# Optimization experiments

Measured on AMD Instinct MI355X. Metric: run time of the kernel, lower is better.

The kernel has to match this reference:

```python
import jax, jax.numpy as jnp
import numpy as np

# Rook contiguity: down, up, right, left
ROOK = ((1, 0), (-1, 0), (0, 1), (0, -1))


def setup_inputs() -> dict:
    key = jax.random.key(0)
    H = W = 2048
    activities = jnp.ones((H, W), dtype=bool)
    vertex_weights = jax.random.uniform(key, (H, W), dtype=jnp.float32)
    return {"activities": activities, "vertex_weights": vertex_weights}


def reference(activities, vertex_weights):
    """Faithful jit-safe translation of GridGraph.get_adjacency_matrix.

    Returns the COO triplet (values, rows, cols) of the adjacency matrix of
    shape (N, N) with N = number of active vertices. All vertices are active
    (activities is all-ones), so N == H*W and the 4*N candidate-edge layout is
    static; invalid edges (out of bounds / inactive target) are masked to
    value 0 at index (0, 0) — an explicit zero, semantically a no-op in COO.
    """
    H, W = activities.shape
    flat = activities.ravel()
    # active_map: passive (i,j) -> active vertex index (== coord_to_active_vertex_index)
    order = jnp.cumsum(flat.astype(jnp.int32)) - 1
    active_map = jnp.where(flat, order, -1).reshape(H, W)
    # source coordinates of active vertices (all active -> full grid, row-major)
    ii, jj = jnp.meshgrid(jnp.arange(H), jnp.arange(W), indexing="ij")
    si, sj = ii.ravel(), jj.ravel()          # [N]
    src_idx = active_map[si, sj]             # [N] == arange(N)

    rows_l, cols_l, vals_l = [], [], []
    for di, dj in ROOK:  # static 4-way loop over neighbor directions
        ci, cj = si + di, sj + dj
        inb = (ci >= 0) & (ci < H) & (cj >= 0) & (cj < W)
        cic = jnp.clip(ci, 0, H - 1)
        cjc = jnp.clip(cj, 0, W - 1)
        valid = inb & activities[cic, cjc]   # edge_validity
        rows_l.append(jnp.where(valid, src_idx, 0))
        cols_l.append(jnp.where(valid, active_map[cic, cjc], 0))
        vals_l.append(jnp.where(valid, vertex_weights[cic, cjc], jnp.float32(0.0)))

    values = jnp.concatenate(vals_l)   # [4N]
    rows = jnp.concatenate(rows_l)     # [4N]
    cols = jnp.concatenate(cols_l)     # [4N]
    return values, rows, cols
```

## Files before the change

kernel.cpp:

```cpp
#include <hip/hip_runtime.h>


constexpr int HH = 2048;
constexpr int WW = 2048;
constexpr long long NN = (long long)HH * WW;

__global__ __launch_bounds__(1024) void grid_adj_kernel(
    const float* __restrict__ w, float* __restrict__ out)
{
    const int t = blockIdx.x * blockDim.x + threadIdx.x;
    const int p = t << 2;
    const int i = p >> 11;
    const int j = p & (WW - 1);

    float* __restrict__ vals = out;
    float* __restrict__ rows = out + 4 * NN;
    float* __restrict__ cols = out + 8 * NN;

    const float fp = (float)p;
    const float4 pf = make_float4(fp, fp + 1.f, fp + 2.f, fp + 3.f);
    const float4 z4 = make_float4(0.f, 0.f, 0.f, 0.f);

    const float4 c0 = *(const float4*)(w + p);

    {
        float4 v = z4, r = z4, c = z4;
        if (i + 1 < HH) {
            v = *(const float4*)(w + p + WW);
            r = pf;
            const float fq = fp + (float)WW;
            c = make_float4(fq, fq + 1.f, fq + 2.f, fq + 3.f);
        }
        *(float4*)(vals + p) = v;
        *(float4*)(rows + p) = r;
        *(float4*)(cols + p) = c;
    }

    {
        float4 v = z4, r = z4, c = z4;
        if (i >= 1) {
            v = *(const float4*)(w + p - WW);
            r = pf;
            const float fq = fp - (float)WW;
            c = make_float4(fq, fq + 1.f, fq + 2.f, fq + 3.f);
        }
        const long long o = NN + p;
        *(float4*)(vals + o) = v;
        *(float4*)(rows + o) = r;
        *(float4*)(cols + o) = c;
    }

    {
        const bool lastok = (j < WW - 4);
        float w4 = 0.f, r3 = 0.f, c3 = 0.f;
        if (lastok) {
            w4 = w[p + 4];
            r3 = fp + 3.f;
            c3 = fp + 4.f;
        }
        const long long o = 2 * NN + p;
        *(float4*)(vals + o) = make_float4(c0.y, c0.z, c0.w, w4);
        *(float4*)(rows + o) = make_float4(pf.x, pf.y, pf.z, r3);
        *(float4*)(cols + o) = make_float4(fp + 1.f, fp + 2.f, fp + 3.f, c3);
    }

    {
        const bool firstok = (j > 0);
        float wm1 = 0.f, r0 = 0.f, c0e = 0.f;
        if (firstok) {
            wm1 = w[p - 1];
            r0 = fp;
            c0e = fp - 1.f;
        }
        const long long o = 3 * NN + p;
        *(float4*)(vals + o) = make_float4(wm1, c0.x, c0.y, c0.z);
        *(float4*)(rows + o) = make_float4(r0, pf.y, pf.z, pf.w);
        *(float4*)(cols + o) = make_float4(c0e, fp, fp + 1.f, fp + 2.f);
    }
}

extern "C" void kernel_launch(void* const* d_in, const int* in_sizes, int n_in,
                              void* d_out, int out_size, void* d_ws, size_t ws_size,
                              hipStream_t stream) {
    const float* w = (const float*)d_in[1];
    float* out = (float*)d_out;

    const int threads = 1024;
    const int total_threads = (int)(NN / 4);
    const int blocks = total_threads / threads;
    grid_adj_kernel<<<blocks, threads, 0, stream>>>(w, out);
}
```

Measured before the change: 213.0 us.

## Assign each block to a single output stream instead of writing all twelve

The kernel is restructured so each block writes one of the twelve output segments (vals, rows and cols for each of four directions), with each thread covering four float4 chunks. Before, every thread wrote to twelve widely separated addresses. Now each wavefront streams contiguously into one region, which is meant to improve DRAM write locality and cut the number of concurrently open streams. In exchange the weight array is re-read by the four value-segment blocks, and the per-segment branching is uniform within a block.

New measurement: 212.1 us. Within noise of the previous version (-0.4%).

```diff
diff --git a/kernel.cpp b/kernel.cpp
--- a/kernel.cpp
+++ b/kernel.cpp
@@ -3,79 +3,67 @@
 
 constexpr int HH = 2048;
 constexpr int WW = 2048;
-constexpr long long NN = (long long)HH * WW;
+constexpr int NN = HH * WW;
 
-__global__ __launch_bounds__(1024) void grid_adj_kernel(
+__global__ __launch_bounds__(1024) void grid_adj_stream(
     const float* __restrict__ w, float* __restrict__ out)
 {
-    const int t = blockIdx.x * blockDim.x + threadIdx.x;
-    const int p = t << 2;
-    const int i = p >> 11;
-    const int j = p & (WW - 1);
+    const int s   = blockIdx.x >> 8;
+    const int blk = blockIdx.x & 255;
+    const int a   = s >> 2;
+    const int d   = s & 3;
+    (void)a;
 
-    float* __restrict__ vals = out;
-    float* __restrict__ rows = out + 4 * NN;
-    float* __restrict__ cols = out + 8 * NN;
+    float* __restrict__ dst = out + (long long)s * NN;
 
-    const float fp = (float)p;
-    const float4 pf = make_float4(fp, fp + 1.f, fp + 2.f, fp + 3.f);
-    const float4 z4 = make_float4(0.f, 0.f, 0.f, 0.f);
+#pragma unroll
+    for (int it = 0; it < 4; ++it) {
+        const int p = ((blk << 2) + it) * 4096 + ((int)threadIdx.x << 2);
+        const int j = p & (WW - 1);
+        const float fp = (float)p;
+        float4 r = make_float4(0.f, 0.f, 0.f, 0.f);
 
-    const float4 c0 = *(const float4*)(w + p);
+        if (d == 0) {
+            if (p < NN - WW) {
+                if (s == 0)      r = *(const float4*)(w + p + WW);
+                else if (s == 4) r = make_float4(fp, fp + 1.f, fp + 2.f, fp + 3.f);
+                else {           const float fq = fp + (float)WW;
+                                 r = make_float4(fq, fq + 1.f, fq + 2.f, fq + 3.f); }
+            }
+        } else if (d == 1) {
+            if (p >= WW) {
+                if (s == 1)      r = *(const float4*)(w + p - WW);
+                else if (s == 5) r = make_float4(fp, fp + 1.f, fp + 2.f, fp + 3.f);
+                else {           const float fq = fp - (float)WW;
+                                 r = make_float4(fq, fq + 1.f, fq + 2.f, fq + 3.f); }
+            }
+        } else if (d == 2) {
+            const bool lastok = (j < WW - 4);
+            if (s == 2) {
+                const float4 c0 = *(const float4*)(w + p);
+                float w4 = 0.f;
+                if (lastok) w4 = w[p + 4];
+                r = make_float4(c0.y, c0.z, c0.w, w4);
+            } else if (s == 6) {
+                r = make_float4(fp, fp + 1.f, fp + 2.f, lastok ? fp + 3.f : 0.f);
+            } else {
+                r = make_float4(fp + 1.f, fp + 2.f, fp + 3.f, lastok ? fp + 4.f : 0.f);
+            }
+        } else {
+            const bool firstok = (j > 0);
+            if (s == 3) {
+                const float4 c0 = *(const float4*)(w + p);
+                float wm1 = 0.f;
+                if (firstok) wm1 = w[p - 1];
+                r = make_float4(wm1, c0.x, c0.y, c0.z);
+            } else if (s == 7) {
+                r = make_float4(firstok ? fp : 0.f, fp + 1.f, fp + 2.f, fp + 3.f);
+            } else {
+                r = make_float4(firstok ? fp - 1.f : 0.f, fp, fp + 1.f, fp + 2.f);
+            }
+        }
 
-    {
-        float4 v = z4, r = z4, c = z4;
-        if (i + 1 < HH) {
-            v = *(const float4*)(w + p + WW);
-            r = pf;
-            const float fq = fp + (float)WW;
-            c = make_float4(fq, fq + 1.f, fq + 2.f, fq + 3.f);
-        }
-        *(float4*)(vals + p) = v;
-        *(float4*)(rows + p) = r;
-        *(float4*)(cols + p) = c;
-    }
-
-    {
-        float4 v = z4, r = z4, c = z4;
-        if (i >= 1) {
-            v = *(const float4*)(w + p - WW);
-            r = pf;
-            const float fq = fp - (float)WW;
-            c = make_float4(fq, fq + 1.f, fq + 2.f, fq + 3.f);
-        }
-        const long long o = NN + p;
-        *(float4*)(vals + o) = v;
-        *(float4*)(rows + o) = r;
-        *(float4*)(cols + o) = c;
-    }
-
-    {
-        const bool lastok = (j < WW - 4);
-        float w4 = 0.f, r3 = 0.f, c3 = 0.f;
-        if (lastok) {
-            w4 = w[p + 4];
-            r3 = fp + 3.f;
-            c3 = fp + 4.f;
-        }
-        const long long o = 2 * NN + p;
-        *(float4*)(vals + o) = make_float4(c0.y, c0.z, c0.w, w4);
-        *(float4*)(rows + o) = make_float4(pf.x, pf.y, pf.z, r3);
-        *(float4*)(cols + o) = make_float4(fp + 1.f, fp + 2.f, fp + 3.f, c3);
-    }
-
-    {
-        const bool firstok = (j > 0);
-        float wm1 = 0.f, r0 = 0.f, c0e = 0.f;
-        if (firstok) {
-            wm1 = w[p - 1];
-            r0 = fp;
-            c0e = fp - 1.f;
-        }
-        const long long o = 3 * NN + p;
-        *(float4*)(vals + o) = make_float4(wm1, c0.x, c0.y, c0.z);
-        *(float4*)(rows + o) = make_float4(r0, pf.y, pf.z, pf.w);
-        *(float4*)(cols + o) = make_float4(c0e, fp, fp + 1.f, fp + 2.f);
+        *(float4*)(dst + p) = r;
     }
 }
 
@@ -86,7 +74,6 @@
     float* out = (float*)d_out;
 
     const int threads = 1024;
-    const int total_threads = (int)(NN / 4);
-    const int blocks = total_threads / threads;
-    grid_adj_kernel<<<blocks, threads, 0, stream>>>(w, out);
+    const int blocks  = 12 * 256;
+    grid_adj_stream<<<blocks, threads, 0, stream>>>(w, out);
 }
```
